# Kernel optimization log

Measured on AMD Instinct MI355X. Metric: run time of the kernel, lower is better.

## Reference

```python
import jax, jax.numpy as jnp
import numpy as np

DIM = 128
DIM_HEAD = 32
HEADS = DIM // DIM_HEAD
WS = 7  # window_size
N = WS ** 3  # tokens per window = 343
TABLE = (2 * WS - 1) ** 3  # 2197


def _rel_pos_indices():
    pos = np.arange(WS)
    grid = np.stack(np.meshgrid(pos, pos, pos, indexing='ij'))  # [3,WS,WS,WS]
    grid = grid.reshape(3, -1).T  # [N,3]
    rel = grid[:, None, :] - grid[None, :, :] + (WS - 1)  # [N,N,3]
    idx = (rel * np.array([(2 * WS - 1) ** 2, 2 * WS - 1, 1])).sum(-1)
    return jnp.asarray(idx, jnp.int32)  # [N,N]


def setup_inputs() -> dict:
    key = jax.random.key(0)
    k1, k2, k3, k4 = jax.random.split(key, 4)
    x = jax.random.normal(k1, (2, 4, 4, 4, WS, WS, WS, DIM), dtype=jnp.float32)
    ln_w = jnp.ones((DIM,), jnp.float32)
    ln_b = jnp.zeros((DIM,), jnp.float32)
    w_qkv = jax.random.normal(k2, (DIM, 3 * DIM), jnp.float32) * 0.02
    w_out = jax.random.normal(k3, (DIM, DIM), jnp.float32) * 0.02
    bias_table = jax.random.normal(k4, (TABLE, HEADS), jnp.float32) * 0.02
    return {"x": x, "ln_w": ln_w, "ln_b": ln_b, "w_qkv": w_qkv,
            "w_out": w_out, "bias_table": bias_table,
            "rel_pos_indices": _rel_pos_indices()}


def reference(x, ln_w, ln_b, w_qkv, w_out, bias_table, rel_pos_indices):
    b, H, W, F, wh, ww, wf, d = x.shape
    scale = DIM_HEAD ** -0.5
    # LayerNorm over last dim (eps=1e-5, torch default)
    mu = x.mean(-1, keepdims=True)
    var = ((x - mu) ** 2).mean(-1, keepdims=True)
    xn = (x - mu) * jax.lax.rsqrt(var + 1e-5) * ln_w + ln_b
    # merge windows: [(b H W F), N, d]
    xr = xn.reshape(-1, wh * ww * wf, d)
    qkv = xr @ w_qkv  # [B, N, 3d]
    q, k, v = jnp.split(qkv, 3, axis=-1)
    def heads(t):
        B, n, _ = t.shape
        return t.reshape(B, n, HEADS, DIM_HEAD).transpose(0, 2, 1, 3)  # [B,h,N,dh]
    q, k, v = heads(q) * scale, heads(k), heads(v)
    sim = jnp.einsum('bhid,bhjd->bhij', q, k)  # [B,h,N,N]
    bias = bias_table[rel_pos_indices]  # [N,N,h]
    sim = sim + bias.transpose(2, 0, 1)[None]  # add [1,h,N,N]
    attn = jax.nn.softmax(sim, axis=-1)
    out = jnp.einsum('bhij,bhjd->bhid', attn, v)  # [B,h,N,dh]
    out = out.transpose(0, 2, 1, 3).reshape(-1, wh * ww * wf, d)
    out = out @ w_out
    return out.reshape(b, H, W, F, wh, ww, wf, d)
```

## Files before the change

kernel.cpp:

```cpp
#include <hip/hip_runtime.h>
#include <cstddef>
#include <cstdint>


#define NTOK 343
#define NPAD 352
#define NT   22
#define LOG2E 1.4426950408889634f
#define QSCALE (0.17677669529663687f * 1.4426950408889634f)

typedef short short8 __attribute__((ext_vector_type(8)));
typedef float f32x4  __attribute__((ext_vector_type(4)));

__device__ __forceinline__ unsigned short f2b(float f) {
    unsigned int u = __float_as_uint(f);
    u = (u + 0x7FFFu + ((u >> 16) & 1u)) >> 16;
    return (unsigned short)u;
}
__device__ __forceinline__ unsigned pk_bf16(float a, float b) {
    unsigned r;
    asm("v_cvt_pk_bf16_f32 %0, %1, %2" : "=v"(r) : "v"(a), "v"(b));
    return r;
}
__device__ __forceinline__ float fast_exp2(float x) {
#if __has_builtin(__builtin_amdgcn_exp2f)
    return __builtin_amdgcn_exp2f(x);
#else
    return exp2f(x);
#endif
}
__device__ __forceinline__ float blo(unsigned u){ return __uint_as_float(u << 16); }
__device__ __forceinline__ float bhi(unsigned u){ return __uint_as_float(u & 0xffff0000u); }

__global__ __launch_bounds__(256) void prep_weights(
    const float* __restrict__ wqkv, const float* __restrict__ wout,
    unsigned short* __restrict__ wqT, unsigned short* __restrict__ woT)
{
    int t = blockIdx.x * 256 + threadIdx.x;
    if (t < 384 * 128) {
        int n = t >> 7, k = t & 127;
        float f = wqkv[k * 384 + n];
        if (n < 128) f *= QSCALE;
        wqT[t] = f2b(f);
    } else {
        int t2 = t - 384 * 128;
        int n = t2 >> 7, k = t2 & 127;
        woT[t2] = f2b(wout[k * 128 + n]);
    }
}

__global__ __launch_bounds__(256) void prep_bias(
    const float* __restrict__ table, const int* __restrict__ rel,
    unsigned short* __restrict__ biasb)
{
    int t = blockIdx.x * 256 + threadIdx.x;
    int r  = t & 3;
    int tp = (t >> 2) & 1;
    int i  = (t >> 3) % NPAD;
    int rest = (t >> 3) / NPAD;
    int g  = rest & 3;  rest >>= 2;
    int c  = rest % 11;
    int h  = rest / 11;
    int j  = (2 * c + tp) * 16 + g * 4 + r;
    float v;
    if (j >= NTOK)      v = -1e30f;
    else if (i >= NTOK) v = 0.0f;
    else                v = table[rel[i * NTOK + j] * 4 + h] * LOG2E;
    biasb[t] = f2b(v);
}

__global__ __launch_bounds__(256) void ln_qkv(
    const float* __restrict__ x, const float* __restrict__ lnw, const float* __restrict__ lnb,
    const unsigned short* __restrict__ wqT,
    unsigned short* __restrict__ qkv_rm)
{
    __shared__ __align__(16) char smem[65536];
    const int by = blockIdx.x, t = threadIdx.x;

    {
        const int r = t >> 1, hf = t & 1;
        const size_t row = (size_t)by * 128 + r;
        const float* src = x + row * 128 + hf * 64;
        float vals[64];
        float s = 0.f, s2 = 0.f;
        #pragma unroll
        for (int c = 0; c < 16; ++c) {
            float4 v = *reinterpret_cast<const float4*>(src + c * 4);
            vals[c*4+0] = v.x; vals[c*4+1] = v.y; vals[c*4+2] = v.z; vals[c*4+3] = v.w;
            s  += v.x + v.y + v.z + v.w;
            s2 += v.x*v.x + v.y*v.y + v.z*v.z + v.w*v.w;
        }
        s  += __shfl_xor(s, 1, 64);
        s2 += __shfl_xor(s2, 1, 64);
        const float mu   = s * (1.f / 128.f);
        const float var  = s2 * (1.f / 128.f) - mu * mu;
        const float rstd = rsqrtf(var + 1e-5f);
        #pragma unroll
        for (int c = 0; c < 8; ++c) {
            unsigned int packed[4];
            #pragma unroll
            for (int e = 0; e < 4; ++e) {
                int idx = c * 8 + e * 2;
                int col = hf * 64 + idx;
                float a = (vals[idx]   - mu) * rstd * lnw[col]   + lnb[col];
                float b = (vals[idx+1] - mu) * rstd * lnw[col+1] + lnb[col+1];
                packed[e] = pk_bf16(a, b);
            }
            int off = (r * 256 + hf * 128 + c * 16) ^ ((r & 7) << 4);
            *reinterpret_cast<int4*>(smem + off) = *reinterpret_cast<const int4*>(packed);
        }
    }

    const int lane = t & 63, wid = t >> 6;
    const int l15 = lane & 15, g = lane >> 4;
    const int wr = wid >> 1, wc = wid & 1;

    for (int sl = 0; sl < 3; ++sl) {
        {
            const int r = t >> 1, hf = t & 1;
            const unsigned short* src = wqT + (size_t)(sl * 128 + r) * 128 + hf * 64;
            #pragma unroll
            for (int c = 0; c < 8; ++c) {
                int4 v = *reinterpret_cast<const int4*>(src + c * 8);
                int off = (r * 256 + hf * 128 + c * 16) ^ ((r & 7) << 4);
                *reinterpret_cast<int4*>(smem + 32768 + off) = v;
            }
        }
        __syncthreads();

        f32x4 acc[4][4] = {};
        #pragma unroll
        for (int ks = 0; ks < 4; ++ks) {
            short8 a[4], b[4];
            #pragma unroll
            for (int mt = 0; mt < 4; ++mt) {
                int row = wr * 64 + mt * 16 + l15;
                int off = (row * 256 + ks * 64 + g * 16) ^ ((row & 7) << 4);
                a[mt] = *reinterpret_cast<const short8*>(smem + off);
            }
            #pragma unroll
            for (int nt = 0; nt < 4; ++nt) {
                int row = wc * 64 + nt * 16 + l15;
                int off = (row * 256 + ks * 64 + g * 16) ^ ((row & 7) << 4);
                b[nt] = *reinterpret_cast<const short8*>(smem + 32768 + off);
            }
            #pragma unroll
            for (int mt = 0; mt < 4; ++mt)
                #pragma unroll
                for (int nt = 0; nt < 4; ++nt)
                    acc[mt][nt] = __builtin_amdgcn_mfma_f32_16x16x32_bf16(a[mt], b[nt], acc[mt][nt], 0, 0, 0);
        }
        __syncthreads();

        #pragma unroll
        for (int mt = 0; mt < 4; ++mt) {
            #pragma unroll
            for (int nt = 0; nt < 4; ++nt) {
                unsigned w01 = pk_bf16(acc[mt][nt][0], acc[mt][nt][1]);
                unsigned w23 = pk_bf16(acc[mt][nt][2], acc[mt][nt][3]);
                int col = wc * 64 + nt * 16 + l15;
                int rb  = wr * 64 + mt * 16 + g * 4;
                unsigned short v4[4] = {(unsigned short)w01, (unsigned short)(w01 >> 16),
                                        (unsigned short)w23, (unsigned short)(w23 >> 16)};
                #pragma unroll
                for (int r4 = 0; r4 < 4; ++r4) {
                    int row = rb + r4;
                    int off = (row * 256 + col * 2) ^ ((row & 28) << 2);
                    *reinterpret_cast<unsigned short*>(smem + 32768 + off) = v4[r4];
                }
            }
        }
        __syncthreads();

        #pragma unroll
        for (int p = 0; p < 8; ++p) {
            int flat = p * 4096 + t * 16;
            int row = flat >> 8, cb = flat & 255;
            int off = (row * 256 + cb) ^ ((row & 28) << 2);
            int4 v = *reinterpret_cast<const int4*>(smem + 32768 + off);
            unsigned token = (unsigned)(by * 128 + row);
            unsigned w = token / 343u;
            unsigned n = token - w * 343u;
            *reinterpret_cast<int4*>(qkv_rm + ((size_t)w * NPAD + n) * 384 + sl * 128 + (cb >> 1)) = v;
        }
        __syncthreads();
    }
}

__global__ __launch_bounds__(256, 3) void attn(
    const unsigned short* __restrict__ qkv_rm, const unsigned short* __restrict__ biasb,
    unsigned short* __restrict__ ao)
{
    __shared__ __align__(16) unsigned short klds[4 * NPAD * 8];
    __shared__ __align__(16) unsigned short vlds[44 * 272];
    __shared__ __align__(16) unsigned short pbuf[4][4][16][8];
    const int bw = blockIdx.x >> 2, h = blockIdx.x & 3;
    const int t = threadIdx.x, lane = t & 63, wid = t >> 6;
    const int l15 = lane & 15, g = lane >> 4;

    const unsigned short* base = qkv_rm + (size_t)bw * NPAD * 384;

    #pragma unroll
    for (int p = 0; p < 11; ++p) {
        int id = p * 256 + t;
        bool isK = id < 1408;
        int id2 = isK ? id : id - 1408;
        int n = id2 >> 2, q4 = id2 & 3;
        const unsigned short* src = base + (size_t)n * 384 + (isK ? 128 : 256) + h * 32 + q4 * 8;
        int4 v = *reinterpret_cast<const int4*>(src);
        if (isK) {
            *reinterpret_cast<int4*>(&klds[(q4 * NPAD + n) * 8]) = v;
        } else {
            const unsigned short* sv = reinterpret_cast<const unsigned short*>(&v);
            int jb = n >> 3, e = n & 7;
            #pragma unroll
            for (int q = 0; q < 8; ++q)
                vlds[jb * 272 + (q4 * 8 + q) * 8 + e] = sv[q];
        }
    }
    __syncthreads();

    const f32x4 zero4 = {0.f, 0.f, 0.f, 0.f};
    for (int it = wid; it < NT; it += 4) {
        const int i = it * 16 + l15;
        short8 qf = *reinterpret_cast<const short8*>(base + (size_t)i * 384 + h * 32 + g * 8);
        short8 bb[11];
        #pragma unroll
        for (int c = 0; c < 11; ++c)
            bb[c] = *reinterpret_cast<const short8*>(biasb + (size_t)(((h * 11 + c) * 4 + g) * NPAD + i) * 8);

        float s = 0.f;
        f32x4 o0 = zero4, o1 = zero4;
        #pragma unroll
        for (int c = 0; c < 11; ++c) {
            short8 kf0 = *reinterpret_cast<const short8*>(&klds[(g * NPAD + 2 * c * 16 + l15) * 8]);
            short8 kf1 = *reinterpret_cast<const short8*>(&klds[(g * NPAD + (2 * c + 1) * 16 + l15) * 8]);
            f32x4 a0 = __builtin_amdgcn_mfma_f32_16x16x32_bf16(kf0, qf, zero4, 0, 0, 0);
            f32x4 a1 = __builtin_amdgcn_mfma_f32_16x16x32_bf16(kf1, qf, zero4, 0, 0, 0);
            const unsigned* bu = reinterpret_cast<const unsigned*>(&bb[c]);
            float p0 = fast_exp2(a0[0] + blo(bu[0]));
            float p1 = fast_exp2(a0[1] + bhi(bu[0]));
            float p2 = fast_exp2(a0[2] + blo(bu[1]));
            float p3 = fast_exp2(a0[3] + bhi(bu[1]));
            float p4 = fast_exp2(a1[0] + blo(bu[2]));
            float p5 = fast_exp2(a1[1] + bhi(bu[2]));
            float p6 = fast_exp2(a1[2] + blo(bu[3]));
            float p7 = fast_exp2(a1[3] + bhi(bu[3]));
            s += ((p0 + p1) + (p2 + p3)) + ((p4 + p5) + (p6 + p7));
            uint2 w0; w0.x = pk_bf16(p0, p1); w0.y = pk_bf16(p2, p3);
            uint2 w1; w1.x = pk_bf16(p4, p5); w1.y = pk_bf16(p6, p7);
            *reinterpret_cast<uint2*>(&pbuf[wid][(g >> 1)][l15][(g & 1) * 4]) = w0;
            *reinterpret_cast<uint2*>(&pbuf[wid][2 + (g >> 1)][l15][(g & 1) * 4]) = w1;
            short8 pf = *reinterpret_cast<const short8*>(&pbuf[wid][g][l15][0]);
            short8 vf0 = *reinterpret_cast<const short8*>(&vlds[(c * 4 + g) * 272 + l15 * 8]);
            short8 vf1 = *reinterpret_cast<const short8*>(&vlds[(c * 4 + g) * 272 + (16 + l15) * 8]);
            o0 = __builtin_amdgcn_mfma_f32_16x16x32_bf16(vf0, pf, o0, 0, 0, 0);
            o1 = __builtin_amdgcn_mfma_f32_16x16x32_bf16(vf1, pf, o1, 0, 0, 0);
        }
        s += __shfl_xor(s, 16, 64);
        s += __shfl_xor(s, 32, 64);
        const float rinv = 1.f / s;

        unsigned short* aorow = ao + ((size_t)bw * NPAD + i) * 128 + h * 32;
        uint2 q0; q0.x = pk_bf16(o0[0] * rinv, o0[1] * rinv); q0.y = pk_bf16(o0[2] * rinv, o0[3] * rinv);
        uint2 q1; q1.x = pk_bf16(o1[0] * rinv, o1[1] * rinv); q1.y = pk_bf16(o1[2] * rinv, o1[3] * rinv);
        *reinterpret_cast<uint2*>(aorow + g * 4) = q0;
        *reinterpret_cast<uint2*>(aorow + 16 + g * 4) = q1;
    }
}

__global__ __launch_bounds__(256) void outproj(
    const unsigned short* __restrict__ ao, const unsigned short* __restrict__ woT,
    float* __restrict__ out)
{
    __shared__ __align__(16) char smem[65536];
    const int t = threadIdx.x;
    const int m0 = blockIdx.x * 128;
    {
        const int r = t >> 1, hf = t & 1;
        const unsigned short* src = ao + (size_t)(m0 + r) * 128 + hf * 64;
        #pragma unroll
        for (int c = 0; c < 8; ++c) {
            int4 v = *reinterpret_cast<const int4*>(src + c * 8);
            int off = (r * 256 + hf * 128 + c * 16) ^ ((r & 7) << 4);
            *reinterpret_cast<int4*>(smem + off) = v;
        }
        const unsigned short* src2 = woT + (size_t)r * 128 + hf * 64;
        #pragma unroll
        for (int c = 0; c < 8; ++c) {
            int4 v = *reinterpret_cast<const int4*>(src2 + c * 8);
            int off = (r * 256 + hf * 128 + c * 16) ^ ((r & 7) << 4);
            *reinterpret_cast<int4*>(smem + 32768 + off) = v;
        }
    }
    __syncthreads();

    const int lane = t & 63, wid = t >> 6;
    const int l15 = lane & 15, g = lane >> 4;
    const int wr = wid >> 1, wc = wid & 1;
    f32x4 acc[4][4] = {};
    #pragma unroll
    for (int ks = 0; ks < 4; ++ks) {
        short8 a[4], b[4];
        #pragma unroll
        for (int mt = 0; mt < 4; ++mt) {
            int row = wr * 64 + mt * 16 + l15;
            int off = (row * 256 + ks * 64 + g * 16) ^ ((row & 7) << 4);
            a[mt] = *reinterpret_cast<const short8*>(smem + off);
        }
        #pragma unroll
        for (int nt = 0; nt < 4; ++nt) {
            int row = wc * 64 + nt * 16 + l15;
            int off = (row * 256 + ks * 64 + g * 16) ^ ((row & 7) << 4);
            b[nt] = *reinterpret_cast<const short8*>(smem + 32768 + off);
        }
        #pragma unroll
        for (int mt = 0; mt < 4; ++mt)
            #pragma unroll
            for (int nt = 0; nt < 4; ++nt)
                acc[mt][nt] = __builtin_amdgcn_mfma_f32_16x16x32_bf16(a[mt], b[nt], acc[mt][nt], 0, 0, 0);
    }
    #pragma unroll
    for (int mt = 0; mt < 4; ++mt) {
        #pragma unroll
        for (int r4 = 0; r4 < 4; ++r4) {
            int row = wr * 64 + mt * 16 + g * 4 + r4;
            unsigned R = (unsigned)(m0 + row);
            unsigned w = R / 352u;
            unsigned n = R - w * 352u;
            if (n < NTOK) {
                float* orow = out + ((size_t)w * NTOK + n) * 128;
                #pragma unroll
                for (int nt = 0; nt < 4; ++nt)
                    orow[wc * 64 + nt * 16 + l15] = acc[mt][nt][r4];
            }
        }
    }
}

extern "C" void kernel_launch(void* const* d_in, const int* in_sizes, int n_in,
                              void* d_out, int out_size, void* d_ws, size_t ws_size,
                              hipStream_t stream)
{
    const float* x     = (const float*)d_in[0];
    const float* lnw   = (const float*)d_in[1];
    const float* lnb   = (const float*)d_in[2];
    const float* wqkv  = (const float*)d_in[3];
    const float* wout  = (const float*)d_in[4];
    const float* table = (const float*)d_in[5];
    const int*   rel   = (const int*)d_in[6];
    float* out = (float*)d_out;

    char* ws = (char*)d_ws;
    unsigned short* qkv_rm = (unsigned short*)(ws + 0);
    unsigned short* ao     = (unsigned short*)(ws + 34603008);
    unsigned short* biasb  = (unsigned short*)(ws + 46137344);
    unsigned short* wqT    = (unsigned short*)(ws + 47128576);
    unsigned short* woT    = (unsigned short*)(ws + 47226880);

    prep_weights<<<256, 256, 0, stream>>>(wqkv, wout, wqT, woT);
    prep_bias<<<1936, 256, 0, stream>>>(table, rel, biasb);
    ln_qkv<<<343, 256, 0, stream>>>(x, lnw, lnb, wqT, qkv_rm);
    attn<<<512, 256, 0, stream>>>(qkv_rm, biasb, ao);
    outproj<<<352, 256, 0, stream>>>(ao, woT, out);
}
```

Measured before the change: 139.9 us.

## Split LayerNorm from QKV GEMM and widen attention blocks to eight waves

LayerNorm now runs as its own kernel that writes pre-swizzled bf16 activations, and the weights are pre-swizzled in the same layout. The QKV projection then runs on a 3x343 grid, one block per output slice, so it has more parallel blocks than the old fused loop over three slices. The attention kernel now uses 512 threads (8 waves) per block with launch bounds (512,4), splitting the query tiles across more waves. The split adds an extra global round-trip for the normalized activations, and the wider attention block may raise register pressure.

```diff
diff --git a/kernel.cpp b/kernel.cpp
--- a/kernel.cpp
+++ b/kernel.cpp
@@ -34,18 +34,19 @@
 
 __global__ __launch_bounds__(256) void prep_weights(
     const float* __restrict__ wqkv, const float* __restrict__ wout,
-    unsigned short* __restrict__ wqT, unsigned short* __restrict__ woT)
+    unsigned short* __restrict__ wqT_sw, unsigned short* __restrict__ woT)
 {
     int t = blockIdx.x * 256 + threadIdx.x;
-    if (t < 384 * 128) {
-        int n = t >> 7, k = t & 127;
-        float f = wqkv[k * 384 + n];
-        if (n < 128) f *= QSCALE;
-        wqT[t] = f2b(f);
+    if (t < 49152) {
+        int s = t >> 14, within = t & 16383;
+        int r = within & 127, k = within >> 7;
+        float f = wqkv[k * 384 + s * 128 + r];
+        if (s == 0) f *= QSCALE;
+        wqT_sw[s * 16384 + ((r * 128 + k) ^ ((r & 7) << 3))] = f2b(f);
     } else {
-        int t2 = t - 384 * 128;
-        int n = t2 >> 7, k = t2 & 127;
-        woT[t2] = f2b(wout[k * 128 + n]);
+        int t2 = t - 49152;
+        int n = t2 & 127, k = t2 >> 7;
+        woT[n * 128 + k] = f2b(wout[k * 128 + n]);
     }
 }
 
@@ -69,131 +70,132 @@
     biasb[t] = f2b(v);
 }
 
-__global__ __launch_bounds__(256) void ln_qkv(
+__global__ __launch_bounds__(256) void ln_x(
     const float* __restrict__ x, const float* __restrict__ lnw, const float* __restrict__ lnb,
-    const unsigned short* __restrict__ wqT,
+    unsigned short* __restrict__ xnsw)
+{
+    const int by = blockIdx.x, t = threadIdx.x;
+    const int r = t >> 1, hf = t & 1;
+    const size_t row = (size_t)by * 128 + r;
+    const float* src = x + row * 128 + hf * 64;
+    char* dst = reinterpret_cast<char*>(xnsw) + (size_t)by * 32768;
+    float vals[64];
+    float s = 0.f, s2 = 0.f;
+    #pragma unroll
+    for (int c = 0; c < 16; ++c) {
+        float4 v = *reinterpret_cast<const float4*>(src + c * 4);
+        vals[c*4+0] = v.x; vals[c*4+1] = v.y; vals[c*4+2] = v.z; vals[c*4+3] = v.w;
+        s  += v.x + v.y + v.z + v.w;
+        s2 += v.x*v.x + v.y*v.y + v.z*v.z + v.w*v.w;
+    }
+    s  += __shfl_xor(s, 1, 64);
+    s2 += __shfl_xor(s2, 1, 64);
+    const float mu   = s * (1.f / 128.f);
+    const float var  = s2 * (1.f / 128.f) - mu * mu;
+    const float rstd = rsqrtf(var + 1e-5f);
+    #pragma unroll
+    for (int c = 0; c < 8; ++c) {
+        unsigned int packed[4];
+        #pragma unroll
+        for (int e = 0; e < 4; ++e) {
+            int idx = c * 8 + e * 2;
+            int col = hf * 64 + idx;
+            float a = (vals[idx]   - mu) * rstd * lnw[col]   + lnb[col];
+            float b = (vals[idx+1] - mu) * rstd * lnw[col+1] + lnb[col+1];
+            packed[e] = pk_bf16(a, b);
+        }
+        int off = (r * 256 + hf * 128 + c * 16) ^ ((r & 7) << 4);
+        *reinterpret_cast<int4*>(dst + off) = *reinterpret_cast<const int4*>(packed);
+    }
+}
+
+__global__ __launch_bounds__(256) void qkv_gemm(
+    const unsigned short* __restrict__ xnsw, const unsigned short* __restrict__ wqT_sw,
     unsigned short* __restrict__ qkv_rm)
 {
     __shared__ __align__(16) char smem[65536];
-    const int by = blockIdx.x, t = threadIdx.x;
+    const int bx = blockIdx.x, by = blockIdx.y, t = threadIdx.x;
 
     {
-        const int r = t >> 1, hf = t & 1;
-        const size_t row = (size_t)by * 128 + r;
-        const float* src = x + row * 128 + hf * 64;
-        float vals[64];
-        float s = 0.f, s2 = 0.f;
-        #pragma unroll
-        for (int c = 0; c < 16; ++c) {
-            float4 v = *reinterpret_cast<const float4*>(src + c * 4);
-            vals[c*4+0] = v.x; vals[c*4+1] = v.y; vals[c*4+2] = v.z; vals[c*4+3] = v.w;
-            s  += v.x + v.y + v.z + v.w;
-            s2 += v.x*v.x + v.y*v.y + v.z*v.z + v.w*v.w;
-        }
-        s  += __shfl_xor(s, 1, 64);
-        s2 += __shfl_xor(s2, 1, 64);
-        const float mu   = s * (1.f / 128.f);
-        const float var  = s2 * (1.f / 128.f) - mu * mu;
-        const float rstd = rsqrtf(var + 1e-5f);
-        #pragma unroll
-        for (int c = 0; c < 8; ++c) {
-            unsigned int packed[4];
-            #pragma unroll
-            for (int e = 0; e < 4; ++e) {
-                int idx = c * 8 + e * 2;
-                int col = hf * 64 + idx;
-                float a = (vals[idx]   - mu) * rstd * lnw[col]   + lnb[col];
-                float b = (vals[idx+1] - mu) * rstd * lnw[col+1] + lnb[col+1];
-                packed[e] = pk_bf16(a, b);
-            }
-            int off = (r * 256 + hf * 128 + c * 16) ^ ((r & 7) << 4);
-            *reinterpret_cast<int4*>(smem + off) = *reinterpret_cast<const int4*>(packed);
-        }
-    }
+        const char* srcA = reinterpret_cast<const char*>(xnsw) + (size_t)by * 32768;
+        const char* srcB = reinterpret_cast<const char*>(wqT_sw) + (size_t)bx * 32768;
+        #pragma unroll
+        for (int p = 0; p < 8; ++p) {
+            int off = p * 4096 + t * 16;
+            *reinterpret_cast<int4*>(smem + off) = *reinterpret_cast<const int4*>(srcA + off);
+            *reinterpret_cast<int4*>(smem + 32768 + off) = *reinterpret_cast<const int4*>(srcB + off);
+        }
+    }
+    __syncthreads();
 
     const int lane = t & 63, wid = t >> 6;
     const int l15 = lane & 15, g = lane >> 4;
     const int wr = wid >> 1, wc = wid & 1;
 
-    for (int sl = 0; sl < 3; ++sl) {
-        {
-            const int r = t >> 1, hf = t & 1;
-            const unsigned short* src = wqT + (size_t)(sl * 128 + r) * 128 + hf * 64;
+    f32x4 acc[4][4] = {};
+    #pragma unroll
+    for (int ks = 0; ks < 4; ++ks) {
+        short8 a[4], b[4];
+        #pragma unroll
+        for (int mt = 0; mt < 4; ++mt) {
+            int row = wr * 64 + mt * 16 + l15;
+            int off = (row * 256 + ks * 64 + g * 16) ^ ((row & 7) << 4);
+            a[mt] = *reinterpret_cast<const short8*>(smem + off);
+        }
+        #pragma unroll
+        for (int nt = 0; nt < 4; ++nt) {
+            int row = wc * 64 + nt * 16 + l15;
+            int off = (row * 256 + ks * 64 + g * 16) ^ ((row & 7) << 4);
+            b[nt] = *reinterpret_cast<const short8*>(smem + 32768 + off);
+        }
+        #pragma unroll
+        for (int mt = 0; mt < 4; ++mt)
             #pragma unroll
-            for (int c = 0; c < 8; ++c) {
-                int4 v = *reinterpret_cast<const int4*>(src + c * 8);
-                int off = (r * 256 + hf * 128 + c * 16) ^ ((r & 7) << 4);
-                *reinterpret_cast<int4*>(smem + 32768 + off) = v;
+            for (int nt = 0; nt < 4; ++nt)
+                acc[mt][nt] = __builtin_amdgcn_mfma_f32_16x16x32_bf16(a[mt], b[nt], acc[mt][nt], 0, 0, 0);
+    }
+    __syncthreads();
+
+    #pragma unroll
+    for (int mt = 0; mt < 4; ++mt) {
+        #pragma unroll
+        for (int nt = 0; nt < 4; ++nt) {
+            unsigned w01 = pk_bf16(acc[mt][nt][0], acc[mt][nt][1]);
+            unsigned w23 = pk_bf16(acc[mt][nt][2], acc[mt][nt][3]);
+            int col = wc * 64 + nt * 16 + l15;
+            int rb  = wr * 64 + mt * 16 + g * 4;
+            unsigned short v4[4] = {(unsigned short)w01, (unsigned short)(w01 >> 16),
+                                    (unsigned short)w23, (unsigned short)(w23 >> 16)};
+            #pragma unroll
+            for (int r4 = 0; r4 < 4; ++r4) {
+                int row = rb + r4;
+                int off = (row * 256 + col * 2) ^ ((row & 28) << 2);
+                *reinterpret_cast<unsigned short*>(smem + off) = v4[r4];
             }
         }
-        __syncthreads();
-
-        f32x4 acc[4][4] = {};
-        #pragma unroll
-        for (int ks = 0; ks < 4; ++ks) {
-            short8 a[4], b[4];
-            #pragma unroll
-            for (int mt = 0; mt < 4; ++mt) {
-                int row = wr * 64 + mt * 16 + l15;
-                int off = (row * 256 + ks * 64 + g * 16) ^ ((row & 7) << 4);
-                a[mt] = *reinterpret_cast<const short8*>(smem + off);
-            }
-            #pragma unroll
-            for (int nt = 0; nt < 4; ++nt) {
-                int row = wc * 64 + nt * 16 + l15;
-                int off = (row * 256 + ks * 64 + g * 16) ^ ((row & 7) << 4);
-                b[nt] = *reinterpret_cast<const short8*>(smem + 32768 + off);
-            }
-            #pragma unroll
-            for (int mt = 0; mt < 4; ++mt)
-                #pragma unroll
-                for (int nt = 0; nt < 4; ++nt)
-                    acc[mt][nt] = __builtin_amdgcn_mfma_f32_16x16x32_bf16(a[mt], b[nt], acc[mt][nt], 0, 0, 0);
-        }
-        __syncthreads();
-
-        #pragma unroll
-        for (int mt = 0; mt < 4; ++mt) {
-            #pragma unroll
-            for (int nt = 0; nt < 4; ++nt) {
-                unsigned w01 = pk_bf16(acc[mt][nt][0], acc[mt][nt][1]);
-                unsigned w23 = pk_bf16(acc[mt][nt][2], acc[mt][nt][3]);
-                int col = wc * 64 + nt * 16 + l15;
-                int rb  = wr * 64 + mt * 16 + g * 4;
-                unsigned short v4[4] = {(unsigned short)w01, (unsigned short)(w01 >> 16),
-                                        (unsigned short)w23, (unsigned short)(w23 >> 16)};
-                #pragma unroll
-                for (int r4 = 0; r4 < 4; ++r4) {
-                    int row = rb + r4;
-                    int off = (row * 256 + col * 2) ^ ((row & 28) << 2);
-                    *reinterpret_cast<unsigned short*>(smem + 32768 + off) = v4[r4];
-                }
-            }
-        }
-        __syncthreads();
-
-        #pragma unroll
-        for (int p = 0; p < 8; ++p) {
-            int flat = p * 4096 + t * 16;
-            int row = flat >> 8, cb = flat & 255;
-            int off = (row * 256 + cb) ^ ((row & 28) << 2);
-            int4 v = *reinterpret_cast<const int4*>(smem + 32768 + off);
-            unsigned token = (unsigned)(by * 128 + row);
-            unsigned w = token / 343u;
-            unsigned n = token - w * 343u;
-            *reinterpret_cast<int4*>(qkv_rm + ((size_t)w * NPAD + n) * 384 + sl * 128 + (cb >> 1)) = v;
-        }
-        __syncthreads();
-    }
-}
-
-__global__ __launch_bounds__(256, 3) void attn(
+    }
+    __syncthreads();
+
+    #pragma unroll
+    for (int p = 0; p < 8; ++p) {
+        int flat = p * 4096 + t * 16;
+        int row = flat >> 8, cb = flat & 255;
+        int off = (row * 256 + cb) ^ ((row & 28) << 2);
+        int4 v = *reinterpret_cast<const int4*>(smem + off);
+        unsigned token = (unsigned)(by * 128 + row);
+        unsigned w = token / 343u;
+        unsigned n = token - w * 343u;
+        *reinterpret_cast<int4*>(qkv_rm + ((size_t)w * NPAD + n) * 384 + bx * 128 + (cb >> 1)) = v;
+    }
+}
+
+__global__ __launch_bounds__(512, 4) void attn(
     const unsigned short* __restrict__ qkv_rm, const unsigned short* __restrict__ biasb,
     unsigned short* __restrict__ ao)
 {
     __shared__ __align__(16) unsigned short klds[4 * NPAD * 8];
     __shared__ __align__(16) unsigned short vlds[44 * 272];
-    __shared__ __align__(16) unsigned short pbuf[4][4][16][8];
+    __shared__ __align__(16) unsigned short pbuf[8][4][16][8];
     const int bw = blockIdx.x >> 2, h = blockIdx.x & 3;
     const int t = threadIdx.x, lane = t & 63, wid = t >> 6;
     const int l15 = lane & 15, g = lane >> 4;
@@ -201,27 +203,29 @@
     const unsigned short* base = qkv_rm + (size_t)bw * NPAD * 384;
 
     #pragma unroll
-    for (int p = 0; p < 11; ++p) {
-        int id = p * 256 + t;
-        bool isK = id < 1408;
-        int id2 = isK ? id : id - 1408;
-        int n = id2 >> 2, q4 = id2 & 3;
-        const unsigned short* src = base + (size_t)n * 384 + (isK ? 128 : 256) + h * 32 + q4 * 8;
-        int4 v = *reinterpret_cast<const int4*>(src);
-        if (isK) {
-            *reinterpret_cast<int4*>(&klds[(q4 * NPAD + n) * 8]) = v;
-        } else {
-            const unsigned short* sv = reinterpret_cast<const unsigned short*>(&v);
-            int jb = n >> 3, e = n & 7;
-            #pragma unroll
-            for (int q = 0; q < 8; ++q)
-                vlds[jb * 272 + (q4 * 8 + q) * 8 + e] = sv[q];
+    for (int p = 0; p < 6; ++p) {
+        int id = p * 512 + t;
+        if (id < 2816) {
+            bool isK = id < 1408;
+            int id2 = isK ? id : id - 1408;
+            int n = id2 >> 2, q4 = id2 & 3;
+            const unsigned short* src = base + (size_t)n * 384 + (isK ? 128 : 256) + h * 32 + q4 * 8;
+            int4 v = *reinterpret_cast<const int4*>(src);
+            if (isK) {
+                *reinterpret_cast<int4*>(&klds[(q4 * NPAD + n) * 8]) = v;
+            } else {
+                const unsigned short* sv = reinterpret_cast<const unsigned short*>(&v);
+                int jb = n >> 3, e = n & 7;
+                #pragma unroll
+                for (int q = 0; q < 8; ++q)
+                    vlds[jb * 272 + (q4 * 8 + q) * 8 + e] = sv[q];
+            }
         }
     }
     __syncthreads();
 
     const f32x4 zero4 = {0.f, 0.f, 0.f, 0.f};
-    for (int it = wid; it < NT; it += 4) {
+    for (int it = wid; it < NT; it += 8) {
         const int i = it * 16 + l15;
         short8 qf = *reinterpret_cast<const short8*>(base + (size_t)i * 384 + h * 32 + g * 8);
         short8 bb[11];
@@ -355,12 +359,14 @@
     unsigned short* qkv_rm = (unsigned short*)(ws + 0);
     unsigned short* ao     = (unsigned short*)(ws + 34603008);
     unsigned short* biasb  = (unsigned short*)(ws + 46137344);
-    unsigned short* wqT    = (unsigned short*)(ws + 47128576);
-    unsigned short* woT    = (unsigned short*)(ws + 47226880);
-
-    prep_weights<<<256, 256, 0, stream>>>(wqkv, wout, wqT, woT);
+    unsigned short* xnsw   = (unsigned short*)(ws + 47128576);
+    unsigned short* wqT_sw = (unsigned short*)(ws + 58368000);
+    unsigned short* woT    = (unsigned short*)(ws + 58466304);
+
+    prep_weights<<<256, 256, 0, stream>>>(wqkv, wout, wqT_sw, woT);
     prep_bias<<<1936, 256, 0, stream>>>(table, rel, biasb);
-    ln_qkv<<<343, 256, 0, stream>>>(x, lnw, lnb, wqT, qkv_rm);
-    attn<<<512, 256, 0, stream>>>(qkv_rm, biasb, ao);
+    ln_x<<<343, 256, 0, stream>>>(x, lnw, lnb, xnsw);
+    qkv_gemm<<<dim3(3, 343), 256, 0, stream>>>(xnsw, wqT_sw, qkv_rm);
+    attn<<<512, 512, 0, stream>>>(qkv_rm, biasb, ao);
     outproj<<<352, 256, 0, stream>>>(ao, woT, out);
 }
```

Result: slower. 144.6 us (+3.4%).
